# Optimization experiments

Hardware: AMD Instinct MI355X
Metric: run time of the kernel (lower is better)

The kernel has to match this reference:

```python
import jax, jax.numpy as jnp
import numpy as np

B, N, C, OUT = 4, 8192, 64, 64
KNN = 36


def knn_point(k, xyz):
    # pairwise squared distances (B,N,N), then k nearest (smallest) indices
    sq = jnp.sum(xyz * xyz, axis=-1)  # (B,N)
    dist = sq[:, :, None] + sq[:, None, :] - 2.0 * jnp.einsum('bnd,bmd->bnm', xyz, xyz)
    _, idx = jax.lax.top_k(-dist, k)  # (B,N,k)
    return idx


def index_points(points, idx):
    # points: (B,N,C), idx: (B,N,K) -> (B,N,K,C)
    return jax.vmap(lambda p, i: p[i])(points, idx)


def setup_inputs() -> dict:
    key = jax.random.key(0)
    ks = jax.random.split(key, 5)
    feature = jax.random.normal(ks[0], (B, N, C), jnp.float32)
    xyz = jax.random.normal(ks[1], (B, N, 3), jnp.float32)
    # linear_v: (input_dim+3) -> out_dim   (stored as (in,out))
    W_v = jax.random.normal(ks[2], (C + 3, OUT), jnp.float32) * 0.05
    b_v = jnp.zeros((OUT,), jnp.float32)
    # suffix_linear: out_dim -> out_dim
    W_suf = jax.random.normal(ks[3], (OUT, OUT), jnp.float32) * 0.05
    b_suf = jnp.zeros((OUT,), jnp.float32)
    return {"feature": feature, "xyz": xyz, "W_v": W_v, "b_v": b_v,
            "W_suf": W_suf, "b_suf": b_suf, "knn_num": KNN}


def reference(feature, xyz, W_v, b_v, W_suf, b_suf, knn_num):
    idx = knn_point(knn_num, xyz)                       # (B,N,K)
    g_f = index_points(feature, idx)                    # (B,N,K,C)
    # weight = g_f @ q[...,None]  -> (B,N,K,1), softmax over K
    w = jnp.einsum('bnkc,bnc->bnk', g_f, feature)
    w = jax.nn.softmax(w, axis=-1)
    # v path: relu(linear_v(cat[feature, xyz]))
    v_feat = jax.nn.relu(jnp.concatenate([feature, xyz], axis=-1) @ W_v + b_v)  # (B,N,OUT)
    group_feature = index_points(v_feat, idx)           # (B,N,K,OUT)
    out = jnp.einsum('bnko,bnk->bno', group_feature, w)  # (B,N,OUT)
    out = out @ W_suf + b_suf
    return (out, N)
```

## Files before the change

### kernel.cpp

```cpp
#include <hip/hip_runtime.h>
#include <stdint.h>
#include <limits.h>

#define BB 4
#define NN 8192
#define CC 64
#define OUTD 64
#define KK 36
#define NPTS (BB * NN)
#define NBIN 129

typedef float v2f __attribute__((ext_vector_type(2)));

static __device__ __forceinline__ int laneid() { return threadIdx.x & 63; }
static __device__ __forceinline__ int waveid_uniform() {
    return __builtin_amdgcn_readfirstlane((int)(threadIdx.x >> 6));
}

__global__ __launch_bounds__(256) void k_vfeat(
    const float* __restrict__ feat, const float* __restrict__ xyz,
    const float* __restrict__ Wv, const float* __restrict__ bv,
    float* __restrict__ vfeat, float4* __restrict__ xyzw)
{
    __shared__ float fb[4][8][64];
    __shared__ float xb[4][8][3];
    const int lane = laneid();
    const int wv = waveid_uniform();
    const int pbase = blockIdx.x * 32 + wv * 8;

    #pragma unroll
    for (int pp = 0; pp < 8; ++pp)
        fb[wv][pp][lane] = feat[(pbase + pp) * CC + lane];
    if (lane < 24)
        xb[wv][lane / 3][lane % 3] = xyz[pbase * 3 + lane];

    const float b0 = bv[lane];
    float acc[8];
    #pragma unroll
    for (int pp = 0; pp < 8; ++pp) acc[pp] = b0;

    #pragma unroll 4
    for (int c = 0; c < CC; ++c) {
        float w = Wv[c * OUTD + lane];
        #pragma unroll
        for (int pp = 0; pp < 8; ++pp)
            acc[pp] = fmaf(fb[wv][pp][c], w, acc[pp]);
    }
    const float wx = Wv[64 * OUTD + lane];
    const float wy = Wv[65 * OUTD + lane];
    const float wz = Wv[66 * OUTD + lane];
    #pragma unroll
    for (int pp = 0; pp < 8; ++pp) {
        float a = acc[pp];
        a = fmaf(xb[wv][pp][0], wx, a);
        a = fmaf(xb[wv][pp][1], wy, a);
        a = fmaf(xb[wv][pp][2], wz, a);
        vfeat[(pbase + pp) * OUTD + lane] = fmaxf(a, 0.0f);
    }
    if (lane < 8) {
        float x = xb[wv][lane][0], y = xb[wv][lane][1], z = xb[wv][lane][2];
        float sq = (x * x + y * y) + z * z;
        xyzw[pbase + lane] = make_float4(x, y, z, sq);
    }
}

__global__ __launch_bounds__(1024) void k_knn(
    const float4* __restrict__ xyzw, int* __restrict__ idx_ws)
{
    __shared__ __align__(16) uint32_t hist[NBIN * 64];
    __shared__ int binB[64];
    __shared__ int cumLoA[64];
    __shared__ uint32_t bufCnt[64];
    __shared__ uint32_t dirCnt[64];

    const int lane = laneid();
    const int wv = waveid_uniform();
    const int batch = blockIdx.x >> 7;
    const int qbase = (blockIdx.x & 127) << 6;
    const int q = qbase + lane;
    const float4* __restrict__ xw = xyzw + batch * NN;

    const float4 Q = xw[q];
    const v2f qx = { Q.x, Q.x };
    const v2f qy = { Q.y, Q.y };
    const v2f qz = { Q.z, Q.z };
    const v2f qw = { Q.w, Q.w };
    const v2f m2 = { -2.0f, -2.0f };

    const int j0 = wv * 512;
    const int laneAdj = lane - 960 * 64;

    for (int i = threadIdx.x; i < NBIN * 64; i += 1024) hist[i] = 0u;
    if (threadIdx.x < 64) { bufCnt[threadIdx.x] = 0u; dirCnt[threadIdx.x] = 0u; }
    __syncthreads();

    #pragma unroll 4
    for (int j = j0; j < j0 + 512; j += 2) {
        float4 C0 = xw[j];
        float4 C1 = xw[j + 1];
        v2f cx = { C0.x, C1.x }, cy = { C0.y, C1.y };
        v2f cz = { C0.z, C1.z }, cw = { C0.w, C1.w };
        v2f dot = __builtin_elementwise_fma(qx, cx,
                  __builtin_elementwise_fma(qy, cy, qz * cz));
        v2f d2  = __builtin_elementwise_fma(m2, dot, qw + cw);
        int t0 = ((int)__float_as_uint(d2.x)) >> 20;
        int t1 = ((int)__float_as_uint(d2.y)) >> 20;
        int m30 = min(max(t0, 960), 1088);
        int m31 = min(max(t1, 960), 1088);
        atomicAdd(&hist[m30 * 64 + laneAdj], 1u);
        atomicAdd(&hist[m31 * 64 + laneAdj], 1u);
    }
    __syncthreads();

    if (threadIdx.x < 64) {
        int cum = 0, Bq = 128, cl = 0;
        for (int b2 = 0; b2 < NBIN; ++b2) {
            int c = (int)hist[b2 * 64 + threadIdx.x];
            if (cum + c >= KK) { Bq = b2; cl = cum; break; }
            cum += c;
        }
        binB[threadIdx.x] = Bq;
        cumLoA[threadIdx.x] = cl;
    }
    __syncthreads();

    const int Bq = binB[lane];
    const int TL = (Bq > 0)    ? (960 + Bq) : INT_MIN;
    const int TH = (Bq == 128) ? INT_MAX    : (960 + Bq);
    const int grow = batch * NN + q;

    unsigned long long* buf = (unsigned long long*)hist;

    #pragma unroll 4
    for (int j = j0; j < j0 + 512; j += 2) {
        float4 C0 = xw[j];
        float4 C1 = xw[j + 1];
        v2f cx = { C0.x, C1.x }, cy = { C0.y, C1.y };
        v2f cz = { C0.z, C1.z }, cw = { C0.w, C1.w };
        v2f dot = __builtin_elementwise_fma(qx, cx,
                  __builtin_elementwise_fma(qy, cy, qz * cz));
        v2f d2  = __builtin_elementwise_fma(m2, dot, qw + cw);
        int t0 = ((int)__float_as_uint(d2.x)) >> 20;
        int t1 = ((int)__float_as_uint(d2.y)) >> 20;
        if (t0 < TL) {
            uint32_t pos = atomicAdd(&dirCnt[lane], 1u);
            idx_ws[grow * KK + (int)pos] = batch * NN + j;
        } else if (t0 <= TH) {
            uint32_t db = __float_as_uint(fmaxf(d2.x, 0.0f));
            uint32_t pos = atomicAdd(&bufCnt[lane], 1u);
            if (pos < 64u) buf[(int)pos * 64 + lane] =
                ((unsigned long long)db << 32) | (uint32_t)j;
        }
        if (t1 < TL) {
            uint32_t pos = atomicAdd(&dirCnt[lane], 1u);
            idx_ws[grow * KK + (int)pos] = batch * NN + (j + 1);
        } else if (t1 <= TH) {
            uint32_t db = __float_as_uint(fmaxf(d2.y, 0.0f));
            uint32_t pos = atomicAdd(&bufCnt[lane], 1u);
            if (pos < 64u) buf[(int)pos * 64 + lane] =
                ((unsigned long long)db << 32) | (uint32_t)(j + 1);
        }
    }
    __syncthreads();

    if (threadIdx.x < 64) {
        const int t = threadIdx.x;
        const int q2 = qbase + t;
        const int grow2 = batch * NN + q2;
        const int cl = cumLoA[t];
        const int r = KK - cl;
        const int M = min((int)bufCnt[t], 64);
        const int outp = grow2 * KK + cl;
        for (int i = 0; i < r; ++i) {
            unsigned long long best = ~0ULL; int bi = -1;
            for (int u = 0; u < M; ++u) {
                unsigned long long v = buf[u * 64 + t];
                if (v < best) { best = v; bi = u; }
            }
            int jj;
            if (bi >= 0) { buf[bi * 64 + t] = ~0ULL; jj = (int)(best & 0xFFFFFFFFu); }
            else jj = q2;
            if (jj < 0 || jj >= NN) jj = q2;
            idx_ws[outp + i] = batch * NN + jj;
        }
    }
}

#define IDX(k) ((((k) & 3) == 0 ? I[(k) >> 2].x : ((k) & 3) == 1 ? I[(k) >> 2].y : \
                 ((k) & 3) == 2 ? I[(k) >> 2].z : I[(k) >> 2].w) & (NPTS - 1))

__global__ __launch_bounds__(256) void k_att(
    const float* __restrict__ feat, const float* __restrict__ vfeat,
    const int* __restrict__ idxw, const float* __restrict__ Wsuf,
    const float* __restrict__ bsuf, float* __restrict__ out)
{
    __shared__ float G[4][KK][33];
    __shared__ float F[4][64];
    __shared__ float Wb[4][KK];
    __shared__ float accb[4][64];
    const int lane = laneid();
    const int wv = waveid_uniform();
    const int p = blockIdx.x * 4 + wv;

    const int4* __restrict__ myidx4 = (const int4*)(idxw + p * KK);
    int4 I[9];
    #pragma unroll
    for (int t = 0; t < 9; ++t) I[t] = myidx4[t];

    const float f = feat[p * CC + lane];
    F[wv][lane] = f;

    const int half = lane >> 5;
    const int cpart = lane & 31;

    float logit = -1e30f;
    float a = 0.0f;
    #pragma unroll
    for (int h = 0; h < 2; ++h) {
        #pragma unroll
        for (int kk = 0; kk < 18; ++kk) {
            int jrow = half ? IDX(2 * kk + 1) : IDX(2 * kk);
            G[wv][2 * kk + half][cpart] = feat[jrow * CC + h * 32 + cpart];
        }
        if (lane < KK) {
            #pragma unroll 8
            for (int c = 0; c < 32; ++c)
                a = fmaf(F[wv][h * 32 + c], G[wv][lane][c], a);
        }
    }
    if (lane < KK) logit = a;

    float m = logit;
    #pragma unroll
    for (int off = 32; off > 0; off >>= 1)
        m = fmaxf(m, __shfl_xor(m, off, 64));
    float e = (lane < KK) ? __expf(logit - m) : 0.0f;
    float s = e;
    #pragma unroll
    for (int off = 32; off > 0; off >>= 1)
        s += __shfl_xor(s, off, 64);
    if (lane < KK) Wb[wv][lane] = e / s;

    float acc = 0.0f;
    #pragma unroll
    for (int k = 0; k < KK; ++k) {
        int j = IDX(k);
        acc = fmaf(Wb[wv][k], vfeat[j * OUTD + lane], acc);
    }
    accb[wv][lane] = acc;

    float o = bsuf[lane];
    #pragma unroll 8
    for (int c = 0; c < OUTD; ++c)
        o = fmaf(accb[wv][c], Wsuf[c * OUTD + lane], o);
    out[p * OUTD + lane] = o;

    if (p == 0 && lane == 0) out[NPTS * OUTD] = (float)NN;
}

extern "C" void kernel_launch(void* const* d_in, const int* in_sizes, int n_in,
                              void* d_out, int out_size, void* d_ws, size_t ws_size,
                              hipStream_t stream)
{
    const float* feat = (const float*)d_in[0];
    const float* xyz  = (const float*)d_in[1];
    const float* Wv   = (const float*)d_in[2];
    const float* bv   = (const float*)d_in[3];
    const float* Wsuf = (const float*)d_in[4];
    const float* bsuf = (const float*)d_in[5];
    float* out = (float*)d_out;

    char* ws = (char*)d_ws;
    float4* xyzw = (float4*)ws;
    float*  vfeat = (float*)(ws + (512 << 10));
    int*    idxw  = (int*)(ws + (512 << 10) + (8 << 20));

    k_vfeat<<<NPTS / 32, 256, 0, stream>>>(feat, xyz, Wv, bv, vfeat, xyzw);
    k_knn  <<<NPTS / 64, 1024, 0, stream>>>(xyzw, idxw);
    k_att  <<<NPTS / 4, 256, 0, stream>>>(feat, vfeat, idxw, Wsuf, bsuf, out);
}
```

Before: 295.9 us.

## Split suffix projection into separate kernel and drop LDS from attention

```diff
diff --git a/kernel.cpp b/kernel.cpp
--- a/kernel.cpp
+++ b/kernel.cpp
@@ -191,13 +191,8 @@
 
 __global__ __launch_bounds__(256) void k_att(
     const float* __restrict__ feat, const float* __restrict__ vfeat,
-    const int* __restrict__ idxw, const float* __restrict__ Wsuf,
-    const float* __restrict__ bsuf, float* __restrict__ out)
-{
-    __shared__ float G[4][KK][33];
-    __shared__ float F[4][64];
-    __shared__ float Wb[4][KK];
-    __shared__ float accb[4][64];
+    const int* __restrict__ idxw, float* __restrict__ outAcc)
+{
     const int lane = laneid();
     const int wv = waveid_uniform();
     const int p = blockIdx.x * 4 + wv;
@@ -207,28 +202,35 @@
     #pragma unroll
     for (int t = 0; t < 9; ++t) I[t] = myidx4[t];
 
-    const float f = feat[p * CC + lane];
-    F[wv][lane] = f;
-
-    const int half = lane >> 5;
-    const int cpart = lane & 31;
-
-    float logit = -1e30f;
+    const int jl = idxw[p * KK + (lane < KK ? lane : 0)] & (NPTS - 1);
+    const float* __restrict__ Gp = feat + (size_t)jl * CC;
+    const float* __restrict__ Fp = feat + (size_t)p * CC;
+
     float a = 0.0f;
     #pragma unroll
-    for (int h = 0; h < 2; ++h) {
-        #pragma unroll
-        for (int kk = 0; kk < 18; ++kk) {
-            int jrow = half ? IDX(2 * kk + 1) : IDX(2 * kk);
-            G[wv][2 * kk + half][cpart] = feat[jrow * CC + h * 32 + cpart];
-        }
-        if (lane < KK) {
-            #pragma unroll 8
-            for (int c = 0; c < 32; ++c)
-                a = fmaf(F[wv][h * 32 + c], G[wv][lane][c], a);
-        }
-    }
-    if (lane < KK) logit = a;
+    for (int ch = 0; ch < 4; ++ch) {
+        const float4 g0 = *(const float4*)(Gp + ch * 16 + 0);
+        const float4 g1 = *(const float4*)(Gp + ch * 16 + 4);
+        const float4 g2 = *(const float4*)(Gp + ch * 16 + 8);
+        const float4 g3 = *(const float4*)(Gp + ch * 16 + 12);
+        a = fmaf(Fp[ch * 16 +  0], g0.x, a);
+        a = fmaf(Fp[ch * 16 +  1], g0.y, a);
+        a = fmaf(Fp[ch * 16 +  2], g0.z, a);
+        a = fmaf(Fp[ch * 16 +  3], g0.w, a);
+        a = fmaf(Fp[ch * 16 +  4], g1.x, a);
+        a = fmaf(Fp[ch * 16 +  5], g1.y, a);
+        a = fmaf(Fp[ch * 16 +  6], g1.z, a);
+        a = fmaf(Fp[ch * 16 +  7], g1.w, a);
+        a = fmaf(Fp[ch * 16 +  8], g2.x, a);
+        a = fmaf(Fp[ch * 16 +  9], g2.y, a);
+        a = fmaf(Fp[ch * 16 + 10], g2.z, a);
+        a = fmaf(Fp[ch * 16 + 11], g2.w, a);
+        a = fmaf(Fp[ch * 16 + 12], g3.x, a);
+        a = fmaf(Fp[ch * 16 + 13], g3.y, a);
+        a = fmaf(Fp[ch * 16 + 14], g3.z, a);
+        a = fmaf(Fp[ch * 16 + 15], g3.w, a);
+    }
+    const float logit = (lane < KK) ? a : -1e30f;
 
     float m = logit;
     #pragma unroll
@@ -239,23 +241,50 @@
     #pragma unroll
     for (int off = 32; off > 0; off >>= 1)
         s += __shfl_xor(s, off, 64);
-    if (lane < KK) Wb[wv][lane] = e / s;
+    const float w = e / s;
 
     float acc = 0.0f;
     #pragma unroll
     for (int k = 0; k < KK; ++k) {
+        float wk = __int_as_float(
+            __builtin_amdgcn_readlane(__float_as_int(w), k));
         int j = IDX(k);
-        acc = fmaf(Wb[wv][k], vfeat[j * OUTD + lane], acc);
-    }
-    accb[wv][lane] = acc;
-
-    float o = bsuf[lane];
-    #pragma unroll 8
-    for (int c = 0; c < OUTD; ++c)
-        o = fmaf(accb[wv][c], Wsuf[c * OUTD + lane], o);
-    out[p * OUTD + lane] = o;
-
-    if (p == 0 && lane == 0) out[NPTS * OUTD] = (float)NN;
+        acc = fmaf(wk, vfeat[j * OUTD + lane], acc);
+    }
+    outAcc[(size_t)p * OUTD + lane] = acc;
+}
+
+__global__ __launch_bounds__(256) void k_proj(
+    const float* __restrict__ Wsuf, const float* __restrict__ bsuf,
+    float* __restrict__ out)
+{
+    const int lane = laneid();
+    const int wv = waveid_uniform();
+    const int pbase = blockIdx.x * 64 + wv * 16;
+    const float bb = bsuf[lane];
+
+    for (int g = 0; g < 4; ++g) {
+        const int p0 = pbase + g * 4;
+        const float* __restrict__ A0 = out + (size_t)(p0 + 0) * OUTD;
+        const float* __restrict__ A1 = out + (size_t)(p0 + 1) * OUTD;
+        const float* __restrict__ A2 = out + (size_t)(p0 + 2) * OUTD;
+        const float* __restrict__ A3 = out + (size_t)(p0 + 3) * OUTD;
+        float o0 = bb, o1 = bb, o2 = bb, o3 = bb;
+        #pragma unroll 8
+        for (int c = 0; c < OUTD; ++c) {
+            const float wc = Wsuf[c * OUTD + lane];
+            o0 = fmaf(A0[c], wc, o0);
+            o1 = fmaf(A1[c], wc, o1);
+            o2 = fmaf(A2[c], wc, o2);
+            o3 = fmaf(A3[c], wc, o3);
+        }
+        out[(size_t)(p0 + 0) * OUTD + lane] = o0;
+        out[(size_t)(p0 + 1) * OUTD + lane] = o1;
+        out[(size_t)(p0 + 2) * OUTD + lane] = o2;
+        out[(size_t)(p0 + 3) * OUTD + lane] = o3;
+    }
+    if (blockIdx.x == 0 && threadIdx.x == 0)
+        out[(size_t)NPTS * OUTD] = (float)NN;
 }
 
 extern "C" void kernel_launch(void* const* d_in, const int* in_sizes, int n_in,
@@ -277,5 +306,6 @@
 
     k_vfeat<<<NPTS / 32, 256, 0, stream>>>(feat, xyz, Wv, bv, vfeat, xyzw);
     k_knn  <<<NPTS / 64, 1024, 0, stream>>>(xyzw, idxw);
-    k_att  <<<NPTS / 4, 256, 0, stream>>>(feat, vfeat, idxw, Wsuf, bsuf, out);
-}
+    k_att  <<<NPTS / 4, 256, 0, stream>>>(feat, vfeat, idxw, out);
+    k_proj <<<NPTS / 64, 256, 0, stream>>>(Wsuf, bsuf, out);
+}
```

After: 322.3 us. +8.9%, slower.
